# Kernel tuning notes

Hardware: AMD Instinct MI355X
Metric: run time of the kernel (lower is better)

The kernel has to match this reference:

```python
import jax, jax.numpy as jnp
import numpy as np

N = 30000
F_IN = 500
HID = 16
OUT = 3
E = 960000


def setup_inputs() -> dict:
    key = jax.random.key(0)
    ks = jax.random.split(key, 10)
    x = jax.random.normal(ks[0], (N, F_IN), dtype=jnp.float32)
    edge_index = jax.random.randint(ks[1], (2, E), 0, N, dtype=jnp.int32)
    # CNN params (torch Conv1d: weight [out, in, k], bias [out])
    s1 = 1.0 / np.sqrt(1 * 3)
    s2 = 1.0 / np.sqrt(HID * 3)
    conv1_w = jax.random.uniform(ks[2], (HID, 1, 3), jnp.float32, -s1, s1)
    conv1_b = jax.random.uniform(ks[3], (HID,), jnp.float32, -s1, s1)
    conv2_w = jax.random.uniform(ks[4], (HID, HID, 3), jnp.float32, -s2, s2)
    conv2_b = jax.random.uniform(ks[5], (HID,), jnp.float32, -s2, s2)
    # GCNConv params (glorot weight [in, out], zero bias)
    g1 = np.sqrt(6.0 / (HID + HID))
    g2 = np.sqrt(6.0 / (HID + OUT))
    gcn1_w = jax.random.uniform(ks[6], (HID, HID), jnp.float32, -g1, g1)
    gcn1_b = jnp.zeros((HID,), jnp.float32)
    gcn2_w = jax.random.uniform(ks[7], (HID, OUT), jnp.float32, -g2, g2)
    gcn2_b = jnp.zeros((OUT,), jnp.float32)
    return {"x": x, "conv1_w": conv1_w, "conv1_b": conv1_b,
            "conv2_w": conv2_w, "conv2_b": conv2_b,
            "gcn1_w": gcn1_w, "gcn1_b": gcn1_b,
            "gcn2_w": gcn2_w, "gcn2_b": gcn2_b,
            "edge_index": edge_index}


def _conv1d(x, w, b):
    # x: [N, C_in, L], w: [C_out, C_in, 3], padding=1
    y = jax.lax.conv_general_dilated(
        x, w, window_strides=(1,), padding=[(1, 1)],
        dimension_numbers=("NCH", "OIH", "NCH"))
    return y + b[None, :, None]


def _gcn_conv(x, w, b, src, dst, n):
    # x: [n, d_in] -> [n, d_out]; Kipf normalization with self-loops
    h = x @ w
    loop = jnp.arange(n, dtype=src.dtype)
    s = jnp.concatenate([src, loop])
    d = jnp.concatenate([dst, loop])
    deg = jax.ops.segment_sum(jnp.ones_like(d, dtype=h.dtype), d, num_segments=n)
    dinv = jnp.where(deg > 0, jax.lax.rsqrt(deg), 0.0)
    norm = dinv[s] * dinv[d]                      # [E+n]
    msg = h[s] * norm[:, None]                    # gather + scale
    return jax.ops.segment_sum(msg, d, num_segments=n) + b


def reference(x, conv1_w, conv1_b, conv2_w, conv2_b,
              gcn1_w, gcn1_b, gcn2_w, gcn2_b, edge_index):
    # CNN feature extractor over feature axis
    h = x[:, None, :]                             # [N, 1, F_IN]
    h = jax.nn.relu(_conv1d(h, conv1_w, conv1_b))  # [N, HID, F_IN]
    h = jax.nn.relu(_conv1d(h, conv2_w, conv2_b))  # [N, HID, F_IN]
    h = jnp.max(h, axis=2)                        # global max pool -> [N, HID]
    # GCN
    src, dst = edge_index[0], edge_index[1]
    n = h.shape[0]
    h = jax.nn.relu(_gcn_conv(h, gcn1_w, gcn1_b, src, dst, n))
    h = _gcn_conv(h, gcn2_w, gcn2_b, src, dst, n)  # [N, OUT]
    return jax.nn.log_softmax(h, axis=1)
```

## Files before the change

### kernel.cpp

```cpp
#include <hip/hip_runtime.h>
#include <hip/hip_bf16.h>

#define N_NODES 30000
#define F_INLEN 500
#define HID 16
#define OUTC 3
#define NEDGE 960000
#define YP 16
#define NBIN 938
#define HBLK 128
#define EPRH (NEDGE / HBLK)
#define ECAP 1536

typedef float  f32x4 __attribute__((ext_vector_type(4)));
typedef float  f32x2 __attribute__((ext_vector_type(2)));
typedef short  s16x8 __attribute__((ext_vector_type(8)));

static __device__ __forceinline__ unsigned short f2bf(float f) {
    unsigned int u = __float_as_uint(f);
    unsigned int r = (u + 0x7fffu + ((u >> 16) & 1u)) >> 16;
    return (unsigned short)r;
}
static __device__ __forceinline__ unsigned int pack_bf16x2(float v0, float v1) {
#if __has_builtin(__builtin_amdgcn_cvt_pk_bf16_f32)
    typedef __bf16 bf16x2_t __attribute__((ext_vector_type(2)));
    union { bf16x2_t v; unsigned int u; } cv;
    cv.v = __builtin_amdgcn_cvt_pk_bf16_f32(v0, v1);
    return cv.u;
#else
    return __builtin_amdgcn_perm(__float_as_uint(v1), __float_as_uint(v0), 0x07060302);
#endif
}

__global__ __launch_bounds__(256) void hist_kernel(
    const float* __restrict__ w2, short* __restrict__ bfragsG,
    const int* __restrict__ dst, int* __restrict__ degi, int* __restrict__ cntbase)
{
    const int tid = threadIdx.x;
    if (blockIdx.x == HBLK) {
        if (tid < 64) {
            const int n16 = tid & 15, q = tid >> 4;
#pragma unroll
            for (int j = 0; j < 8; j++) {
                {
                    const int c = q * 8 + j;
                    const int t = c >> 4, i = c & 15;
                    bfragsG[tid * 16 + j] = (short)f2bf(w2[n16 * 48 + i * 3 + t]);
                }
                {
                    const int c = 32 + q * 8 + j;
                    short v = 0;
                    if (c < 48) { const int t = c >> 4, i = c & 15; v = (short)f2bf(w2[n16 * 48 + i * 3 + t]); }
                    bfragsG[tid * 16 + 8 + j] = v;
                }
            }
        }
        return;
    }
    __shared__ int histH[NBIN];
    for (int i = tid; i < NBIN; i += 256) histH[i] = 0;
    __syncthreads();
    const int e0 = blockIdx.x * EPRH;
    for (int e = e0 + tid; e < e0 + EPRH; e += 256) {
        const int d = dst[e];
        atomicAdd(&histH[d >> 5], 1);
        atomicAdd(&degi[d], 1);
    }
    __syncthreads();
    for (int i = tid; i < NBIN; i += 256) cntbase[blockIdx.x * NBIN + i] = histH[i];
}

__global__ __launch_bounds__(256, 8) void conv_reorder(
    const float* __restrict__ x,
    const float* __restrict__ w1, const float* __restrict__ b1,
    const float* __restrict__ b2, const short* __restrict__ bfragsG,
    const int* __restrict__ src, const int* __restrict__ dst,
    const int* __restrict__ degi, const int* __restrict__ cntbase,
    int* __restrict__ packed, int* __restrict__ binstart,
    float* __restrict__ h0)
{
    __shared__ __align__(16) unsigned short yh[516 * YP];
    __shared__ __align__(16) float xp[502];
    __shared__ float red[64];

    const int tid = threadIdx.x;

    if (blockIdx.x < HBLK) {
        int* scA    = (int*)yh;
        int* scB    = scA + NBIN;
        int* totb   = scB + NBIN;
        int* cursor = totb + NBIN;
        const int blk = blockIdx.x;
        for (int bin = tid; bin < NBIN; bin += 256) {
            int tot = 0, psum = 0;
            for (int k = 0; k < HBLK; k++) {
                const int c = cntbase[k * NBIN + bin];
                tot += c;
                if (k < blk) psum += c;
            }
            scA[bin]    = tot;
            totb[bin]   = tot;
            cursor[bin] = psum;
        }
        __syncthreads();
        int* pA = scA; int* pB = scB;
        for (int off = 1; off < NBIN; off <<= 1) {
            for (int i = tid; i < NBIN; i += 256)
                pB[i] = pA[i] + ((i >= off) ? pA[i - off] : 0);
            __syncthreads();
            int* tp = pA; pA = pB; pB = tp;
        }
        for (int i = tid; i < NBIN; i += 256) {
            const int excl = pA[i] - totb[i];
            cursor[i] += excl;
            if (blk == 0) binstart[i] = excl;
        }
        if (blk == 0 && tid == 0) binstart[NBIN] = NEDGE;
        __syncthreads();
        const int e0 = blk * EPRH;
        for (int e = e0 + tid; e < e0 + EPRH; e += 256) {
            const int d = dst[e];
            const int pos = atomicAdd(&cursor[d >> 5], 1);
            packed[pos] = src[e] | (d << 15);
        }
        return;
    }

    const int node = blockIdx.x - HBLK;
    const int dgi  = degi[node];
    const int lane = tid & 63;
    const int wave = tid >> 6;
    const int n16  = lane & 15;
    const int q    = lane >> 4;

    if (tid == 0) { xp[0] = 0.f; xp[501] = 0.f; }
    if (tid < 125) {
        const float4 v = ((const float4*)(x + (long long)node * F_INLEN))[tid];
        xp[4 * tid + 1] = v.x; xp[4 * tid + 2] = v.y;
        xp[4 * tid + 3] = v.z; xp[4 * tid + 4] = v.w;
    }
    {
        const int ri = tid >> 4;
        const int row = (ri == 0) ? 0 : (500 + ri);
        yh[row * YP + (tid & 15)] = 0;
    }
    const s16x8* bfp = (const s16x8*)(bfragsG + lane * 16);
    const s16x8 bh0 = bfp[0], bh1 = bfp[1];

    f32x2 wt0[8], wt1[8], wt2[8], bbv[8];
#pragma unroll
    for (int cp = 0; cp < 8; cp++) {
        const int c0 = 2 * cp, c1 = 2 * cp + 1;
        wt0[cp] = (f32x2){w1[c0 * 3 + 0], w1[c1 * 3 + 0]};
        wt1[cp] = (f32x2){w1[c0 * 3 + 1], w1[c1 * 3 + 1]};
        wt2[cp] = (f32x2){w1[c0 * 3 + 2], w1[c1 * 3 + 2]};
        bbv[cp] = (f32x2){b1[c0], b1[c1]};
    }
    __syncthreads();

    for (int p = tid; p < 500; p += 256) {
        const float x0 = xp[p], x1 = xp[p + 1], x2 = xp[p + 2];
        const f32x2 xv0 = {x0, x0}, xv1 = {x1, x1}, xv2 = {x2, x2};
        const f32x2 zero = {0.f, 0.f};
        unsigned int hp[8];
#pragma unroll
        for (int cp = 0; cp < 8; cp++) {
            f32x2 a = __builtin_elementwise_fma(wt0[cp], xv0, bbv[cp]);
            a = __builtin_elementwise_fma(wt1[cp], xv1, a);
            a = __builtin_elementwise_fma(wt2[cp], xv2, a);
            a = __builtin_elementwise_max(a, zero);
            hp[cp] = pack_bf16x2(a[0], a[1]);
        }
        uint4* d = (uint4*)&yh[(p + 1) * YP];
        d[0] = make_uint4(hp[0], hp[1], hp[2], hp[3]);
        d[1] = make_uint4(hp[4], hp[5], hp[6], hp[7]);
    }
    __syncthreads();

    const unsigned short* ybase = yh + (n16 + (q >> 1)) * YP + (q & 1) * 8
                                     + wave * (8 * 16 * YP);
    f32x4 mxv = {-3.0e38f, -3.0e38f, -3.0e38f, -3.0e38f};
    f32x4 mxt = {-3.0e38f, -3.0e38f, -3.0e38f, -3.0e38f};
#pragma unroll
    for (int it = 0; it < 8; it++) {
        const s16x8 ah0 = *(const s16x8*)(ybase + it * (16 * YP));
        const s16x8 ah1 = *(const s16x8*)(ybase + it * (16 * YP) + 2 * YP);
        f32x4 acc = {0.f, 0.f, 0.f, 0.f};
        acc = __builtin_amdgcn_mfma_f32_16x16x32_bf16(ah0, bh0, acc, 0, 0, 0);
        acc = __builtin_amdgcn_mfma_f32_16x16x32_bf16(ah1, bh1, acc, 0, 0, 0);
        if (it < 7) mxv = __builtin_elementwise_max(mxv, acc);
        else        mxt = __builtin_elementwise_max(mxt, acc);
    }
    if (wave < 3 || q == 0) mxv = __builtin_elementwise_max(mxv, mxt);
    float m = fmaxf(fmaxf(mxv[0], mxv[1]), fmaxf(mxv[2], mxv[3]));
    m = fmaxf(m, __shfl_xor(m, 16));
    m = fmaxf(m, __shfl_xor(m, 32));
    if (lane < 16) red[wave * 16 + lane] = m;
    __syncthreads();
    if (tid < 16) {
        const float mm = fmaxf(fmaxf(red[tid], red[16 + tid]), fmaxf(red[32 + tid], red[48 + tid]));
        const float dv = rsqrtf((float)(dgi + 1));
        h0[node * HID + tid] = fmaxf(mm + b2[tid], 0.f) * dv;
    }
}

__global__ __launch_bounds__(512) void agg1_kernel(
    const int* __restrict__ binstart, int* __restrict__ packed,
    const float* __restrict__ h0,
    const float* __restrict__ W1, const float* __restrict__ b1g,
    const float* __restrict__ W2, float4* __restrict__ t2p4,
    int* __restrict__ binofs)
{
    __shared__ float w1s[256];
    __shared__ float w2s[48];
    __shared__ float b1s[16];
    __shared__ float accS[32 * 17];
    __shared__ int eL[ECAP];
    __shared__ int srt[ECAP];
    __shared__ int h32[32], ls32[32], lofs32[32];
    const int tid = threadIdx.x;
    const int blk = blockIdx.x;
    if (tid < 256) w1s[tid] = W1[tid];
    if (tid < 48) w2s[tid] = W2[tid];
    if (tid < 16) b1s[tid] = b1g[tid];
    if (tid < 32) h32[tid] = 0;
    const int beg = binstart[blk];
    const int cnt = binstart[blk + 1] - beg;
    __syncthreads();
    for (int j = tid; j < cnt; j += 512) {
        const int p = packed[beg + j];
        eL[j] = p;
        atomicAdd(&h32[(p >> 15) & 31], 1);
    }
    __syncthreads();
    if (tid < 32) {
        const int v = h32[tid];
        int inc = v;
#pragma unroll
        for (int off = 1; off < 32; off <<= 1) {
            const int y = __shfl_up(inc, off);
            if (tid >= off) inc += y;
        }
        ls32[tid] = inc - v;
        lofs32[tid] = inc - v;
    }
    __syncthreads();
    for (int j = tid; j < cnt; j += 512) {
        const int p = eL[j];
        const int pos = atomicAdd(&lofs32[(p >> 15) & 31], 1);
        srt[pos] = p;
    }
    __syncthreads();
    for (int j = tid; j < cnt; j += 512) packed[beg + j] = srt[j];
    if (tid < 32) {
        binofs[blk * 64 + tid]      = ls32[tid];
        binofs[blk * 64 + 32 + tid] = h32[tid];
    }
    const int n = tid >> 4;
    const int eslot = (tid >> 2) & 3;
    const int q = tid & 3;
    const int node = blk * 32 + n;
    const bool valid = node < N_NODES;
    f32x4 acc = {0.f, 0.f, 0.f, 0.f};
    if (valid) {
        const int s0 = ls32[n];
        const int s1 = s0 + h32[n];
        for (int i = s0 + eslot; i < s1; i += 4) {
            const int s = srt[i] & 32767;
            acc += *(const f32x4*)(h0 + s * HID + q * 4);
        }
    }
#pragma unroll
    for (int c = 0; c < 4; c++) {
        acc[c] += __shfl_xor(acc[c], 4);
        acc[c] += __shfl_xor(acc[c], 8);
    }
    if (valid && eslot == 0) {
        acc += *(const f32x4*)(h0 + node * HID + q * 4);
        accS[n * 17 + q * 4 + 0] = acc[0];
        accS[n * 17 + q * 4 + 1] = acc[1];
        accS[n * 17 + q * 4 + 2] = acc[2];
        accS[n * 17 + q * 4 + 3] = acc[3];
    }
    __syncthreads();
    if (tid < 128) {
        const int n2 = tid >> 2;
        const int node2 = blk * 32 + n2;
        if (node2 < N_NODES) {
            const float dv = rsqrtf((float)(h32[n2] + 1));
            const int q2 = tid & 3;
            float y0 = 0.f, y1 = 0.f, y2 = 0.f, y3 = 0.f;
#pragma unroll
            for (int i = 0; i < 16; i++) {
                const float a = accS[n2 * 17 + i];
                y0 = fmaf(a, w1s[i * 16 + q2 * 4 + 0], y0);
                y1 = fmaf(a, w1s[i * 16 + q2 * 4 + 1], y1);
                y2 = fmaf(a, w1s[i * 16 + q2 * 4 + 2], y2);
                y3 = fmaf(a, w1s[i * 16 + q2 * 4 + 3], y3);
            }
            float d0 = 0.f, d1 = 0.f, d2 = 0.f;
            const float yv[4] = {y0, y1, y2, y3};
#pragma unroll
            for (int j = 0; j < 4; j++) {
                const int o = q2 * 4 + j;
                const float h = fmaxf(b1s[o] + dv * yv[j], 0.f);
                d0 = fmaf(h, w2s[o * 3 + 0], d0);
                d1 = fmaf(h, w2s[o * 3 + 1], d1);
                d2 = fmaf(h, w2s[o * 3 + 2], d2);
            }
            d0 += __shfl_xor(d0, 1); d0 += __shfl_xor(d0, 2);
            d1 += __shfl_xor(d1, 1); d1 += __shfl_xor(d1, 2);
            d2 += __shfl_xor(d2, 1); d2 += __shfl_xor(d2, 2);
            if (q2 == 0) t2p4[node2] = make_float4(d0 * dv, d1 * dv, d2 * dv, dv);
        }
    }
}

__global__ __launch_bounds__(512) void agg2_kernel(
    const int* __restrict__ binstart, const int* __restrict__ packed,
    const float4* __restrict__ t2p4, const int* __restrict__ binofs,
    const float* __restrict__ b2g, float* __restrict__ out)
{
    __shared__ int eL[ECAP];
    __shared__ int ofs[64];
    const int tid = threadIdx.x;
    const int blk = blockIdx.x;
    const int beg = binstart[blk];
    const int cnt = binstart[blk + 1] - beg;
    if (tid < 64) ofs[tid] = binofs[blk * 64 + tid];
    for (int j = tid; j < cnt; j += 512) eL[j] = packed[beg + j];
    __syncthreads();
    const int n = tid >> 4;
    const int ln16 = tid & 15;
    const int node = blk * 32 + n;
    float a0 = 0.f, a1 = 0.f, a2 = 0.f;
    if (node < N_NODES) {
        const int s0 = ofs[n];
        const int s1 = s0 + ofs[32 + n];
        for (int i = s0 + ln16; i < s1; i += 16) {
            const int s = eL[i] & 32767;
            const float4 v = t2p4[s];
            a0 += v.x; a1 += v.y; a2 += v.z;
        }
    }
#pragma unroll
    for (int msk = 1; msk < 16; msk <<= 1) {
        a0 += __shfl_xor(a0, msk);
        a1 += __shfl_xor(a1, msk);
        a2 += __shfl_xor(a2, msk);
    }
    if (ln16 == 0 && node < N_NODES) {
        const float4 self = t2p4[node];
        const float dv = self.w;
        const float z0 = b2g[0] + dv * (a0 + self.x);
        const float z1 = b2g[1] + dv * (a1 + self.y);
        const float z2 = b2g[2] + dv * (a2 + self.z);
        const float m = fmaxf(z0, fmaxf(z1, z2));
        const float lg = m + logf(expf(z0 - m) + expf(z1 - m) + expf(z2 - m));
        out[node * 3 + 0] = z0 - lg;
        out[node * 3 + 1] = z1 - lg;
        out[node * 3 + 2] = z2 - lg;
    }
}

extern "C" void kernel_launch(void* const* d_in, const int* in_sizes, int n_in,
                              void* d_out, int out_size, void* d_ws, size_t ws_size,
                              hipStream_t stream)
{
    const float* x   = (const float*)d_in[0];
    const float* w1  = (const float*)d_in[1];
    const float* b1  = (const float*)d_in[2];
    const float* w2  = (const float*)d_in[3];
    const float* b2  = (const float*)d_in[4];
    const float* g1w = (const float*)d_in[5];
    const float* g1b = (const float*)d_in[6];
    const float* g2w = (const float*)d_in[7];
    const float* g2b = (const float*)d_in[8];
    const int*   ei  = (const int*)d_in[9];
    const int* src = ei;
    const int* dst = ei + NEDGE;

    float* ws = (float*)d_ws;
    float*  h0      = ws;
    float4* t2p4    = (float4*)(ws + 480000);
    int*    degi    = (int*)(ws + 600000);
    int*    cntbase = (int*)(ws + 630000);
    int*    binstart= (int*)(ws + 750064);
    int*    packed  = (int*)(ws + 751104);
    int*    binofs  = (int*)(ws + 1711104);
    short*  bfragsG = (short*)(ws + 1771136);
    float*  out     = (float*)d_out;

    hipMemsetAsync(degi, 0, N_NODES * sizeof(int), stream);
    hist_kernel<<<HBLK + 1, 256, 0, stream>>>(w2, bfragsG, dst, degi, cntbase);
    conv_reorder<<<HBLK + N_NODES, 256, 0, stream>>>(x, w1, b1, b2, bfragsG,
                                                     src, dst, degi, cntbase,
                                                     packed, binstart, h0);
    agg1_kernel<<<NBIN, 512, 0, stream>>>(binstart, packed, h0,
                                          g1w, g1b, g2w, t2p4, binofs);
    agg2_kernel<<<NBIN, 512, 0, stream>>>(binstart, packed, t2p4, binofs, g2b, out);
}
```

Measured before the change: 213.9 us.

## Make conv blocks persistent over node ranges with double-buffered x prefetch

Replaces the one-block-per-node conv launch (30000 blocks) with 1664 persistent blocks that each loop over a contiguous range of nodes. The next node's input row and degree are loaded into a second shared-memory buffer while the current node's conv and MFMA max-pool run. Per-block setup (weights, B fragments, bias, padding rows) is now paid once per block rather than once per node. This costs an extra __syncthreads per node and lowers the occupancy hint from 8 to 7, and boundary padding is now done with conditionals in the inner loop.

```diff
diff --git a/kernel.cpp b/kernel.cpp
--- a/kernel.cpp
+++ b/kernel.cpp
@@ -9,6 +9,7 @@
 #define YP 16
 #define NBIN 938
 #define HBLK 128
+#define NCONV 1664
 #define EPRH (NEDGE / HBLK)
 #define ECAP 1536
 
@@ -70,7 +71,7 @@
     for (int i = tid; i < NBIN; i += 256) cntbase[blockIdx.x * NBIN + i] = histH[i];
 }
 
-__global__ __launch_bounds__(256, 8) void conv_reorder(
+__global__ __launch_bounds__(256, 7) void conv_reorder(
     const float* __restrict__ x,
     const float* __restrict__ w1, const float* __restrict__ b1,
     const float* __restrict__ b2, const short* __restrict__ bfragsG,
@@ -79,8 +80,8 @@
     int* __restrict__ packed, int* __restrict__ binstart,
     float* __restrict__ h0)
 {
-    __shared__ __align__(16) unsigned short yh[516 * YP];
-    __shared__ __align__(16) float xp[502];
+    __shared__ __align__(16) unsigned short yh[515 * YP];
+    __shared__ __align__(16) float xp2[2][500];
     __shared__ float red[64];
 
     const int tid = threadIdx.x;
@@ -126,23 +127,22 @@
         return;
     }
 
-    const int node = blockIdx.x - HBLK;
-    const int dgi  = degi[node];
+    const int cb   = blockIdx.x - HBLK;
+    const int base = N_NODES / NCONV;
+    const int rem  = N_NODES % NCONV;
+    const int n0   = cb * base + (cb < rem ? cb : rem);
+    const int ncnt = base + (cb < rem ? 1 : 0);
+
     const int lane = tid & 63;
     const int wave = tid >> 6;
     const int n16  = lane & 15;
     const int q    = lane >> 4;
 
-    if (tid == 0) { xp[0] = 0.f; xp[501] = 0.f; }
-    if (tid < 125) {
-        const float4 v = ((const float4*)(x + (long long)node * F_INLEN))[tid];
-        xp[4 * tid + 1] = v.x; xp[4 * tid + 2] = v.y;
-        xp[4 * tid + 3] = v.z; xp[4 * tid + 4] = v.w;
-    }
-    {
-        const int ri = tid >> 4;
-        const int row = (ri == 0) ? 0 : (500 + ri);
-        yh[row * YP + (tid & 15)] = 0;
+    if (tid < 240) {
+        int row, col;
+        if (tid < 16) { row = 0; col = tid; }
+        else { row = 501 + (tid - 16) / 16; col = (tid - 16) & 15; }
+        yh[row * YP + col] = 0;
     }
     const s16x8* bfp = (const s16x8*)(bfragsG + lane * 16);
     const s16x8 bh0 = bfp[0], bh1 = bfp[1];
@@ -156,51 +156,78 @@
         wt2[cp] = (f32x2){w1[c0 * 3 + 2], w1[c1 * 3 + 2]};
         bbv[cp] = (f32x2){b1[c0], b1[c1]};
     }
-    __syncthreads();
-
-    for (int p = tid; p < 500; p += 256) {
-        const float x0 = xp[p], x1 = xp[p + 1], x2 = xp[p + 2];
-        const f32x2 xv0 = {x0, x0}, xv1 = {x1, x1}, xv2 = {x2, x2};
-        const f32x2 zero = {0.f, 0.f};
-        unsigned int hp[8];
-#pragma unroll
-        for (int cp = 0; cp < 8; cp++) {
-            f32x2 a = __builtin_elementwise_fma(wt0[cp], xv0, bbv[cp]);
-            a = __builtin_elementwise_fma(wt1[cp], xv1, a);
-            a = __builtin_elementwise_fma(wt2[cp], xv2, a);
-            a = __builtin_elementwise_max(a, zero);
-            hp[cp] = pack_bf16x2(a[0], a[1]);
-        }
-        uint4* d = (uint4*)&yh[(p + 1) * YP];
-        d[0] = make_uint4(hp[0], hp[1], hp[2], hp[3]);
-        d[1] = make_uint4(hp[4], hp[5], hp[6], hp[7]);
-    }
-    __syncthreads();
+    const float b2v = (tid < 16) ? b2[tid] : 0.f;
+
+    if (tid < 125) {
+        const float4 v = ((const float4*)(x + (long long)n0 * F_INLEN))[tid];
+        *((float4*)&xp2[0][tid * 4]) = v;
+    }
+    int dgn = degi[n0];
+    int cur = 0;
 
     const unsigned short* ybase = yh + (n16 + (q >> 1)) * YP + (q & 1) * 8
                                      + wave * (8 * 16 * YP);
-    f32x4 mxv = {-3.0e38f, -3.0e38f, -3.0e38f, -3.0e38f};
-    f32x4 mxt = {-3.0e38f, -3.0e38f, -3.0e38f, -3.0e38f};
-#pragma unroll
-    for (int it = 0; it < 8; it++) {
-        const s16x8 ah0 = *(const s16x8*)(ybase + it * (16 * YP));
-        const s16x8 ah1 = *(const s16x8*)(ybase + it * (16 * YP) + 2 * YP);
-        f32x4 acc = {0.f, 0.f, 0.f, 0.f};
-        acc = __builtin_amdgcn_mfma_f32_16x16x32_bf16(ah0, bh0, acc, 0, 0, 0);
-        acc = __builtin_amdgcn_mfma_f32_16x16x32_bf16(ah1, bh1, acc, 0, 0, 0);
-        if (it < 7) mxv = __builtin_elementwise_max(mxv, acc);
-        else        mxt = __builtin_elementwise_max(mxt, acc);
-    }
-    if (wave < 3 || q == 0) mxv = __builtin_elementwise_max(mxv, mxt);
-    float m = fmaxf(fmaxf(mxv[0], mxv[1]), fmaxf(mxv[2], mxv[3]));
-    m = fmaxf(m, __shfl_xor(m, 16));
-    m = fmaxf(m, __shfl_xor(m, 32));
-    if (lane < 16) red[wave * 16 + lane] = m;
-    __syncthreads();
-    if (tid < 16) {
-        const float mm = fmaxf(fmaxf(red[tid], red[16 + tid]), fmaxf(red[32 + tid], red[48 + tid]));
-        const float dv = rsqrtf((float)(dgi + 1));
-        h0[node * HID + tid] = fmaxf(mm + b2[tid], 0.f) * dv;
+
+    for (int i = 0; i < ncnt; ++i) {
+        const int n = n0 + i;
+        float4 pf;
+        const bool hp = (i + 1 < ncnt) && (tid < 125);
+        if (hp) pf = ((const float4*)(x + (long long)(n + 1) * F_INLEN))[tid];
+        const int dgnext = (i + 1 < ncnt) ? degi[n + 1] : 0;
+
+        __syncthreads();
+
+        const float* xc = xp2[cur];
+        for (int p = tid; p < 500; p += 256) {
+            const float xm = (p > 0)   ? xc[p - 1] : 0.f;
+            const float x0 = xc[p];
+            const float xr = (p < 499) ? xc[p + 1] : 0.f;
+            const f32x2 xv0 = {xm, xm}, xv1 = {x0, x0}, xv2 = {xr, xr};
+            const f32x2 zero = {0.f, 0.f};
+            unsigned int hpk[8];
+#pragma unroll
+            for (int cp = 0; cp < 8; cp++) {
+                f32x2 a = __builtin_elementwise_fma(wt0[cp], xv0, bbv[cp]);
+                a = __builtin_elementwise_fma(wt1[cp], xv1, a);
+                a = __builtin_elementwise_fma(wt2[cp], xv2, a);
+                a = __builtin_elementwise_max(a, zero);
+                hpk[cp] = pack_bf16x2(a[0], a[1]);
+            }
+            uint4* d = (uint4*)&yh[(p + 1) * YP];
+            d[0] = make_uint4(hpk[0], hpk[1], hpk[2], hpk[3]);
+            d[1] = make_uint4(hpk[4], hpk[5], hpk[6], hpk[7]);
+        }
+        __syncthreads();
+
+        f32x4 mxv = {-3.0e38f, -3.0e38f, -3.0e38f, -3.0e38f};
+        f32x4 mxt = {-3.0e38f, -3.0e38f, -3.0e38f, -3.0e38f};
+#pragma unroll
+        for (int it = 0; it < 8; it++) {
+            const s16x8 ah0 = *(const s16x8*)(ybase + it * (16 * YP));
+            const s16x8 ah1 = *(const s16x8*)(ybase + it * (16 * YP) + 2 * YP);
+            f32x4 acc = {0.f, 0.f, 0.f, 0.f};
+            acc = __builtin_amdgcn_mfma_f32_16x16x32_bf16(ah0, bh0, acc, 0, 0, 0);
+            acc = __builtin_amdgcn_mfma_f32_16x16x32_bf16(ah1, bh1, acc, 0, 0, 0);
+            if (it < 7) mxv = __builtin_elementwise_max(mxv, acc);
+            else        mxt = __builtin_elementwise_max(mxt, acc);
+        }
+        if (wave < 3 || q == 0) mxv = __builtin_elementwise_max(mxv, mxt);
+        float m = fmaxf(fmaxf(mxv[0], mxv[1]), fmaxf(mxv[2], mxv[3]));
+        m = fmaxf(m, __shfl_xor(m, 16));
+        m = fmaxf(m, __shfl_xor(m, 32));
+        if (lane < 16) red[wave * 16 + lane] = m;
+
+        if (hp) *((float4*)&xp2[cur ^ 1][tid * 4]) = pf;
+
+        __syncthreads();
+        if (tid < 16) {
+            const float mm = fmaxf(fmaxf(red[tid], red[16 + tid]),
+                                   fmaxf(red[32 + tid], red[48 + tid]));
+            const float dv = rsqrtf((float)(dgn + 1));
+            h0[n * HID + tid] = fmaxf(mm + b2v, 0.f) * dv;
+        }
+        dgn = dgnext;
+        cur ^= 1;
     }
 }
 
@@ -393,9 +420,9 @@
 
     hipMemsetAsync(degi, 0, N_NODES * sizeof(int), stream);
     hist_kernel<<<HBLK + 1, 256, 0, stream>>>(w2, bfragsG, dst, degi, cntbase);
-    conv_reorder<<<HBLK + N_NODES, 256, 0, stream>>>(x, w1, b1, b2, bfragsG,
-                                                     src, dst, degi, cntbase,
-                                                     packed, binstart, h0);
+    conv_reorder<<<HBLK + NCONV, 256, 0, stream>>>(x, w1, b1, b2, bfragsG,
+                                                   src, dst, degi, cntbase,
+                                                   packed, binstart, h0);
     agg1_kernel<<<NBIN, 512, 0, stream>>>(binstart, packed, h0,
                                           g1w, g1b, g2w, t2p4, binofs);
     agg2_kernel<<<NBIN, 512, 0, stream>>>(binstart, packed, t2p4, binofs, g2b, out);
```

Result: slower. 223.7 us (+4.6%).
